# Kernel tuning notes

Hardware: AMD Instinct MI355X
Metric: run time of the kernel (lower is better)

Reference implementation:

```python
import jax, jax.numpy as jnp
import numpy as np

# Marching-tetrahedra lookup tables (identical to the torch module).
_TRI_TABLE = np.array([
    [-1,-1,-1,-1,-1,-1],[1,0,2,-1,-1,-1],[4,0,3,-1,-1,-1],[1,4,2,1,3,4],
    [3,1,5,-1,-1,-1],[2,3,0,2,5,3],[1,4,0,1,5,4],[4,2,5,-1,-1,-1],
    [4,5,2,-1,-1,-1],[4,1,0,4,5,1],[3,2,0,3,5,2],[1,3,5,-1,-1,-1],
    [4,1,2,4,3,1],[3,0,4,-1,-1,-1],[2,0,1,-1,-1,-1],[-1,-1,-1,-1,-1,-1]], dtype=np.int64)
_NUM_TRI = np.array([0,1,1,2,1,2,2,1,1,2,2,1,2,1,1,0], dtype=np.int64)
_BASE_EDGES = np.array([0,1,0,2,0,3,1,2,1,3,2,3], dtype=np.int64)
_NUM_TETS = np.array([0,1,1,3,1,3,3,3,1,3,3,3,3,3,3,1], dtype=np.int64)
_TET_TABLE = np.array([
    [-1,-1,-1,-1,-1,-1,-1,-1,-1,-1,-1,-1],[0,4,5,6,-1,-1,-1,-1,-1,-1,-1,-1],
    [1,4,8,7,-1,-1,-1,-1,-1,-1,-1,-1],[7,1,8,6,5,1,7,6,5,0,1,6],
    [2,5,7,9,-1,-1,-1,-1,-1,-1,-1,-1],[4,0,6,7,9,0,7,6,7,0,9,2],
    [4,1,9,8,5,1,9,4,5,1,2,9],[6,0,1,2,8,6,1,2,9,6,8,2],
    [3,6,9,8,-1,-1,-1,-1,-1,-1,-1,-1],[5,0,4,8,5,0,8,3,5,8,9,3],
    [1,4,7,3,4,7,6,3,9,6,7,3],[0,1,5,3,5,1,9,3,5,1,7,9],
    [5,2,3,7,3,6,5,8,3,5,7,8],[0,4,7,8,0,3,8,7,0,3,7,2],
    [4,1,2,3,4,3,2,5,4,3,5,6],[0,1,2,3,-1,-1,-1,-1,-1,-1,-1,-1]], dtype=np.int64)


def _precompute(n_verts, sdf, tet, thickness):
    """Integer / no_grad half of DMTet.__call__ (dynamic shapes -> host numpy)."""
    sdf = np.asarray(sdf)
    tet = np.asarray(tet).astype(np.int64)
    th = float(np.asarray(thickness).reshape(-1)[0])
    occ = (sdf > 0) & (sdf <= th)                      # [N]
    occ_f = occ[tet]                                   # [F,4]
    occ_sum = occ_f.sum(-1)
    valid = (occ_sum > 0) & (occ_sum < 4)
    vt = tet[valid]                                    # [V,4] surface tets
    edges = vt[:, _BASE_EDGES].reshape(-1, 2)          # [V*6,2]
    edges = np.sort(edges, axis=1)                     # == sort_edges
    uniq, inv = np.unique(edges, axis=0, return_inverse=True)
    inv = inv.reshape(-1)
    mask_e = occ[uniq].sum(-1) == 1                    # crossing edges
    mapping = np.full(uniq.shape[0], -1, dtype=np.int64)
    mapping[mask_e] = np.arange(int(mask_e.sum()), dtype=np.int64)
    idx_map = mapping[inv].reshape(-1, 6)              # [V,6]
    interp_v = uniq[mask_e]                            # [E,2]
    ti = (occ_f[valid].astype(np.int64) * np.array([1, 2, 4, 8])).sum(-1)  # tetindex
    nt = _NUM_TRI[ti]
    f1 = np.take_along_axis(idx_map[nt == 1], _TRI_TABLE[ti[nt == 1]][:, :3], axis=1).reshape(-1, 3)
    f2 = np.take_along_axis(idx_map[nt == 2], _TRI_TABLE[ti[nt == 2]][:, :6], axis=1).reshape(-1, 3)
    faces = np.concatenate([f1, f2], axis=0)
    ntt = _NUM_TETS[ti]
    tve = np.concatenate([vt, idx_map + n_verts], axis=1)  # [V,10]: 4 verts + 6 edge-verts
    t1 = np.take_along_axis(tve[ntt == 1], _TET_TABLE[ti[ntt == 1]][:, :4], axis=1).reshape(-1, 4)
    t3 = np.take_along_axis(tve[ntt == 3], _TET_TABLE[ti[ntt == 3]][:, :12], axis=1).reshape(-1, 4)
    inner = tet[occ_sum == 4]
    all_tets = np.concatenate([t1, t3, inner], axis=0)
    all_unique, inv2 = np.unique(all_tets.reshape(-1), return_inverse=True)
    tets_tetmesh = inv2.reshape(-1, 4)
    return interp_v, faces, all_unique, tets_tetmesh


def _interp(pos, sdf, th, interp_v, all_unique_tets):
    """Differentiable half: edge interpolation + gather of tetmesh verts."""
    e = pos[interp_v.reshape(-1)].reshape(-1, 2, 3)    # [E,2,3]
    s = sdf[interp_v.reshape(-1)].reshape(-1, 2, 1)    # [E,2,1]
    both_pos = (s[:, 0, 0] > 0) & (s[:, 1, 0] > 0)
    s = jnp.where(both_pos[:, None, None], s - th, s)  # shift band edges
    s = s * jnp.array([1.0, -1.0], dtype=s.dtype)[None, :, None]  # negate 2nd
    denom = s.sum(axis=1, keepdims=True)
    w = jnp.flip(s, axis=1) / denom                    # linear interp weights
    verts = (e * w).sum(axis=1)                        # [E,3]
    all_verts = jnp.concatenate([pos, verts], axis=0)
    verts_tetmesh = all_verts[all_unique_tets]
    return verts, verts_tetmesh


def setup_inputs() -> dict:
    key = jax.random.key(0)
    k1, k2, k3, k4 = jax.random.split(key, 4)
    N, F = 400000, 2000000
    pos_nx3 = jax.random.normal(k1, (N, 3), dtype=jnp.float32)
    sdf_n = jax.random.normal(k2, (N,), dtype=jnp.float32)
    tet_fx4 = jax.random.randint(k3, (F, 4), 0, N, dtype=jnp.int32)
    thickness = jax.random.uniform(k4, (1,), dtype=jnp.float32, minval=0.3, maxval=0.8)
    return {"pos_nx3": pos_nx3, "sdf_n": sdf_n, "tet_fx4": tet_fx4, "thickness": thickness}


def reference(pos_nx3, sdf_n, tet_fx4, thickness):
    interp_v, faces, all_unique, tets_tm = _precompute(pos_nx3.shape[0], sdf_n, tet_fx4, thickness)
    verts, verts_tetmesh = _interp(pos_nx3, sdf_n, thickness[0], jnp.asarray(interp_v), jnp.asarray(all_unique))
    return verts, jnp.asarray(faces), verts_tetmesh, jnp.asarray(tets_tm)
```

## Files before the change

kernel.cpp:

```cpp
#include <hip/hip_runtime.h>
#include <stdint.h>

typedef unsigned int u32;
typedef unsigned long long u64;

__device__ __constant__ int c_TRI[16][6] = {
 {-1,-1,-1,-1,-1,-1},{1,0,2,-1,-1,-1},{4,0,3,-1,-1,-1},{1,4,2,1,3,4},
 {3,1,5,-1,-1,-1},{2,3,0,2,5,3},{1,4,0,1,5,4},{4,2,5,-1,-1,-1},
 {4,5,2,-1,-1,-1},{4,1,0,4,5,1},{3,2,0,3,5,2},{1,3,5,-1,-1,-1},
 {4,1,2,4,3,1},{3,0,4,-1,-1,-1},{2,0,1,-1,-1,-1},{-1,-1,-1,-1,-1,-1}};
__device__ __constant__ int c_NTRI[16] = {0,1,1,2,1,2,2,1,1,2,2,1,2,1,1,0};
__device__ __constant__ int c_NTET[16] = {0,1,1,3,1,3,3,3,1,3,3,3,3,3,3,1};
__device__ __constant__ int c_TET[16][12] = {
 {-1,-1,-1,-1,-1,-1,-1,-1,-1,-1,-1,-1},{0,4,5,6,-1,-1,-1,-1,-1,-1,-1,-1},
 {1,4,8,7,-1,-1,-1,-1,-1,-1,-1,-1},{7,1,8,6,5,1,7,6,5,0,1,6},
 {2,5,7,9,-1,-1,-1,-1,-1,-1,-1,-1},{4,0,6,7,9,0,7,6,7,0,9,2},
 {4,1,9,8,5,1,9,4,5,1,2,9},{6,0,1,2,8,6,1,2,9,6,8,2},
 {3,6,9,8,-1,-1,-1,-1,-1,-1,-1,-1},{5,0,4,8,5,0,8,3,5,8,9,3},
 {1,4,7,3,4,7,6,3,9,6,7,3},{0,1,5,3,5,1,9,3,5,1,7,9},
 {5,2,3,7,3,6,5,8,3,5,7,8},{0,4,7,8,0,3,8,7,0,3,7,2},
 {4,1,2,3,4,3,2,5,4,3,5,6},{0,1,2,3,-1,-1,-1,-1,-1,-1,-1,-1}};
__device__ __constant__ int c_EV[12] = {0,1,0,2,0,3,1,2,1,3,2,3};

#define GSLOOP(i,n) for (long long i = (long long)blockIdx.x*blockDim.x + threadIdx.x; \
                         i < (long long)(n); i += (long long)gridDim.x*blockDim.x)

__global__ __launch_bounds__(256) void k_scan1(u32* data, u32* partials,
                                               const u32* hdr, int nslot, u32 nmax) {
  __shared__ u32 lds[2048];
  __shared__ u32 tsum[256];
  u32 n = (nslot >= 0) ? hdr[nslot] : nmax;
  u32 base = blockIdx.x * 2048u;
  for (int k = threadIdx.x; k < 2048; k += 256) {
    u32 i = base + (u32)k;
    lds[k] = (i < n) ? data[i] : 0u;
  }
  __syncthreads();
  u32 o = threadIdx.x * 8u;
  u32 run = 0; u32 loc[8];
  #pragma unroll
  for (int j = 0; j < 8; j++) { loc[j] = run; run += lds[o + j]; }
  tsum[threadIdx.x] = run;
  __syncthreads();
  for (int off = 1; off < 256; off <<= 1) {
    u32 v = tsum[threadIdx.x];
    u32 add = (threadIdx.x >= (u32)off) ? tsum[threadIdx.x - off] : 0u;
    __syncthreads();
    tsum[threadIdx.x] = v + add;
    __syncthreads();
  }
  u32 texc = (threadIdx.x == 0) ? 0u : tsum[threadIdx.x - 1];
  #pragma unroll
  for (int j = 0; j < 8; j++) {
    u32 i = base + o + (u32)j;
    if (i < n) data[i] = texc + loc[j];
  }
  if (threadIdx.x == 0) partials[blockIdx.x] = tsum[255];
}

__global__ __launch_bounds__(1024) void k_scan2(u32* partials, const u32* hdr, int nslot,
                                                u32 nmax, u32* hdrw, int tslot) {
  __shared__ u32 lds[8192];
  __shared__ u32 tsum[1024];
  u32 n = (nslot >= 0) ? hdr[nslot] : nmax;
  u32 nb = (n + 2047u) / 2048u;
  for (int k = threadIdx.x; k < 8192; k += 1024) lds[k] = ((u32)k < nb) ? partials[k] : 0u;
  __syncthreads();
  u32 o = threadIdx.x * 8u;
  u32 run = 0; u32 loc[8];
  #pragma unroll
  for (int j = 0; j < 8; j++) { loc[j] = run; run += lds[o + j]; }
  tsum[threadIdx.x] = run;
  __syncthreads();
  for (int off = 1; off < 1024; off <<= 1) {
    u32 v = tsum[threadIdx.x];
    u32 add = (threadIdx.x >= (u32)off) ? tsum[threadIdx.x - off] : 0u;
    __syncthreads();
    tsum[threadIdx.x] = v + add;
    __syncthreads();
  }
  u32 texc = (threadIdx.x == 0) ? 0u : tsum[threadIdx.x - 1];
  #pragma unroll
  for (int j = 0; j < 8; j++) { u32 k = o + (u32)j; if (k < nb) partials[k] = texc + loc[j]; }
  if (threadIdx.x == 0 && tslot >= 0) hdrw[tslot] = tsum[1023];
}

__global__ __launch_bounds__(256) void k_scan3(u32* data, const u32* partials,
                                               const u32* hdr, int nslot, u32 nmax) {
  u32 n = (nslot >= 0) ? hdr[nslot] : nmax;
  u32 base = blockIdx.x * 2048u;
  if (base >= n || blockIdx.x == 0) return;
  u32 add = partials[blockIdx.x];
  if (add == 0) return;
  for (int k = threadIdx.x; k < 2048; k += 256) {
    u32 i = base + (u32)k;
    if (i < n) data[i] += add;
  }
}

__global__ void k_zero32(u32* p, long long n) { GSLOOP(i, n) p[i] = 0u; }
__global__ void k_zero_hdr(u32* p, const u32* hdr, int slot, u32 extra) {
  long long n = (long long)hdr[slot] + extra;
  GSLOOP(i, n) p[i] = 0u;
}
__global__ void k_copy32(const u32* s, u32* d, long long n) { GSLOOP(i, n) d[i] = s[i]; }
__global__ void k_setr(u32* hdr, int N) { hdr[10] = (u32)N + hdr[3]; }

__global__ void k_occ(const float* sdf, const float* th, unsigned char* occ, int N) {
  float t = th[0];
  GSLOOP(i, N) { float s = sdf[i]; occ[i] = (s > 0.f && s <= t) ? 1 : 0; }
}

__global__ void k_ti(const int* tet, const unsigned char* occ, unsigned char* ti,
                     u32* S1, long long F) {
  GSLOOP(f, F) {
    int v0 = tet[4*f], v1 = tet[4*f+1], v2 = tet[4*f+2], v3 = tet[4*f+3];
    int b = (int)occ[v0] | ((int)occ[v1] << 1) | ((int)occ[v2] << 2) | ((int)occ[v3] << 3);
    ti[f] = (unsigned char)b;
    S1[f] = (b != 0 && b != 15) ? 1u : 0u;
  }
}

__global__ void k_compact_valid(const u32* S1, const unsigned char* ti, u32* vidx, long long F) {
  GSLOOP(f, F) { int b = ti[f]; if (b != 0 && b != 15) vidx[S1[f]] = (u32)f; }
}

__global__ void k_hist(const int* tet, const u32* vidx, const u32* hdr, u32* hist) {
  u32 V = hdr[0];
  GSLOOP(t, V) {
    long long f = vidx[t];
    int v[4] = { tet[4*f], tet[4*f+1], tet[4*f+2], tet[4*f+3] };
    #pragma unroll
    for (int e = 0; e < 6; e++) {
      int a = v[c_EV[2*e]], b = v[c_EV[2*e+1]];
      int mn = a < b ? a : b;
      atomicAdd(&hist[mn], 1u);
    }
  }
}

__global__ void k_bnd(const u32* off, u32* hdr, int N) {
  int g = threadIdx.x;
  if (g > 8) return;
  if (g == 8) { hdr[16 + 8] = (u32)N; return; }
  u64 target = ((u64)hdr[1] * (u64)g) / 8ull;
  u32 lo = 0, hi = (u32)N;
  while (lo < hi) { u32 m = (lo + hi) >> 1; if ((u64)off[m] < target) lo = m + 1; else hi = m; }
  hdr[16 + g] = lo;
}

__global__ void k_scatter8(const int* tet, const u32* vidx, const u32* hdr,
                           u32* cursor, u64* keys, int SB, int OB) {
  int g = blockIdx.x & 7;
  u32 lo = hdr[16 + g], hi = hdr[16 + g + 1];
  u32 V = hdr[0];
  for (long long t = (long long)(blockIdx.x >> 3) * blockDim.x + threadIdx.x; t < (long long)V;
       t += (long long)(gridDim.x >> 3) * blockDim.x) {
    long long f = vidx[t];
    int v[4] = { tet[4*f], tet[4*f+1], tet[4*f+2], tet[4*f+3] };
    #pragma unroll
    for (int e = 0; e < 6; e++) {
      int a = v[c_EV[2*e]], b = v[c_EV[2*e+1]];
      int mn = a < b ? a : b, mx = a < b ? b : a;
      if ((u32)mn >= lo && (u32)mn < hi) {
        u32 p = atomicAdd(&cursor[mn], 1u);
        keys[p] = (((u64)(u32)mn << (SB + OB)) | ((u64)(u32)mx << OB)) | (u64)(6ull * t + e);
      }
    }
  }
}

template<int KMAX>
__device__ __forceinline__ void bitonic_lane(u64& val, int lane) {
  #pragma unroll
  for (int k = 2; k <= KMAX; k <<= 1) {
    #pragma unroll
    for (int j = k >> 1; j > 0; j >>= 1) {
      u64 other = __shfl_xor(val, j, 64);
      bool keepmin = ((lane & k) == 0) == ((lane & j) == 0);
      bool smaller = val < other;
      val = (keepmin == smaller) ? val : other;
    }
  }
}

__global__ __launch_bounds__(256) void k_bsort(const u32* off, u64* keys, u32* cfe,
                                               const unsigned char* occm, int N,
                                               int SB, int OB) {
  int lane = threadIdx.x & 63;
  u64 smask = ((u64)1 << SB) - 1;
  long long wid = ((long long)blockIdx.x * blockDim.x + threadIdx.x) >> 6;
  long long nw  = ((long long)gridDim.x * blockDim.x) >> 6;
  for (long long v = wid; v < N; v += nw) {
    u32 s = off[v], e = off[v + 1];
    u32 cnt = e - s;
    if (cnt == 0) continue;
    int ov = (int)occm[v];
    if (cnt == 1) {
      if (lane == 0) {
        u32 mx = (u32)((keys[s] >> OB) & smask);
        cfe[s] = ((ov + (int)occm[mx]) == 1) ? 1u : 0u;
      }
      continue;
    }
    if (cnt <= 64) {
      u64 val = (lane < (int)cnt) ? keys[s + lane] : ~0ull;
      if      (cnt <= 2)  bitonic_lane<2>(val, lane);
      else if (cnt <= 4)  bitonic_lane<4>(val, lane);
      else if (cnt <= 8)  bitonic_lane<8>(val, lane);
      else if (cnt <= 16) bitonic_lane<16>(val, lane);
      else if (cnt <= 32) bitonic_lane<32>(val, lane);
      else                bitonic_lane<64>(val, lane);
      u64 prev = __shfl_up(val, 1, 64);
      if (lane < (int)cnt) {
        keys[s + lane] = val;
        bool flag = (lane == 0) || ((val >> OB) != (prev >> OB));
        u32 mx = (u32)((val >> OB) & smask);
        cfe[s + lane] = (flag && ((ov + (int)occm[mx]) == 1)) ? 1u : 0u;
      }
    } else if (cnt <= 256) {
      u64 vals[4];
      #pragma unroll
      for (int r = 0; r < 4; r++) {
        int idx = r * 64 + lane;
        vals[r] = (idx < (int)cnt) ? keys[s + idx] : ~0ull;
      }
      #pragma unroll
      for (int k = 2; k <= 256; k <<= 1) {
        #pragma unroll
        for (int j = 128; j > 0; j >>= 1) {
          if (j >= k) continue;
          if (j >= 64) {
            int rj = j >> 6;
            #pragma unroll
            for (int r = 0; r < 4; r++) {
              int pr = r ^ rj;
              if (pr > r) {
                int i0 = r * 64 + lane;
                bool keepmin = ((i0 & k) == 0);
                u64 a = vals[r], b = vals[pr];
                u64 mn = a < b ? a : b, mx = a < b ? b : a;
                vals[r]  = keepmin ? mn : mx;
                vals[pr] = keepmin ? mx : mn;
              }
            }
          } else {
            #pragma unroll
            for (int r = 0; r < 4; r++) {
              int i0 = r * 64 + lane;
              u64 other = __shfl_xor(vals[r], j, 64);
              bool keepmin = ((i0 & k) == 0) == ((i0 & j) == 0);
              bool smaller = vals[r] < other;
              vals[r] = (keepmin == smaller) ? vals[r] : other;
            }
          }
        }
      }
      #pragma unroll
      for (int r = 0; r < 4; r++) {
        u64 pv = __shfl_up(vals[r], 1, 64);
        u64 lastprev = (r > 0) ? __shfl(vals[r - 1], 63, 64) : 0ull;
        int idx = r * 64 + lane;
        u64 prev = (lane == 0) ? lastprev : pv;
        if (idx < (int)cnt) {
          keys[s + idx] = vals[r];
          bool flag = (idx == 0) || ((vals[r] >> OB) != (prev >> OB));
          u32 mx = (u32)((vals[r] >> OB) & smask);
          cfe[s + idx] = (flag && ((ov + (int)occm[mx]) == 1)) ? 1u : 0u;
        }
      }
    } else if (lane == 0) {
      for (u32 i = s + 1; i < e; i++) {
        u64 kk = keys[i]; u32 j = i;
        while (j > s && keys[j - 1] > kk) { keys[j] = keys[j - 1]; j--; }
        keys[j] = kk;
      }
      for (u32 j = s; j < e; j++) {
        bool flag = (j == s) || ((keys[j] >> OB) != (keys[j - 1] >> OB));
        u32 mx = (u32)((keys[j] >> OB) & smask);
        cfe[j] = (flag && ((ov + (int)occm[mx]) == 1)) ? 1u : 0u;
      }
    }
  }
}

__global__ void k_idxscatter8(const u64* keys, const u32* S, const unsigned char* occm,
                              int* idx_map, u64* ie, const u32* hdr, int SB, int OB) {
  u32 E = hdr[1];
  int g = blockIdx.x & 7;
  u64 omask = ((u64)1 << OB) - 1;
  u64 smask = ((u64)1 << SB) - 1;
  for (long long i = (long long)(blockIdx.x >> 3) * blockDim.x + threadIdx.x; i < (long long)E;
       i += (long long)(gridDim.x >> 3) * blockDim.x) {
    u64 k = keys[i];
    u32 oidx = (u32)(k & omask);
    u32 mx = (u32)((k >> OB) & smask);
    u32 mn = (u32)(k >> (SB + OB));
    bool flag = (i == 0) || ((k >> OB) != (keys[i - 1] >> OB));
    bool cf = ((int)occm[mn] + (int)occm[mx]) == 1;
    u32 sv = S[i];
    int mapval = cf ? (int)(flag ? sv : sv - 1u) : -1;
    u32 slice = (u32)(((u64)oidx * 8ull) / (u64)E);
    if (slice == (u32)g) idx_map[oidx] = mapval;
    if (g == 0 && flag && cf) ie[sv] = ((u64)mn << 32) | (u64)mx;
  }
}

__global__ void k_interp(const u64* ie, const float* pos, const float* sdf,
                         const float* th, float* out, const u32* hdr) {
  u32 EC = hdr[3];
  float t = th[0];
  GSLOOP(m, EC) {
    u64 k = ie[m]; int a = (int)(k >> 32), b = (int)(k & 0xffffffffu);
    float s0 = sdf[a], s1 = sdf[b];
    if (s0 > 0.f && s1 > 0.f) { s0 = __fsub_rn(s0, t); s1 = __fsub_rn(s1, t); }
    float denom = __fadd_rn(s0, -s1);
    float w0 = __fdiv_rn(-s1, denom);
    float w1 = __fdiv_rn(s0, denom);
    long long base = 3ll * m;
    #pragma unroll
    for (int kk = 0; kk < 3; kk++)
      out[base + kk] = __fadd_rn(__fmul_rn(pos[3ll*a + kk], w0), __fmul_rn(pos[3ll*b + kk], w1));
  }
}

__global__ void k_pred_faces(const unsigned char* ti, u32* S1, u32* S2, long long F) {
  GSLOOP(f, F) {
    int b = ti[f]; bool valid = (b != 0 && b != 15); int nt = c_NTRI[b];
    S1[f] = (valid && nt == 1) ? 1u : 0u;
    S2[f] = (valid && nt == 2) ? 1u : 0u;
  }
}

__global__ void k_faces(const u32* vidx, const unsigned char* ti, const int* idx_map,
                        const u32* S1, const u32* S2, float* out, const u32* hdr) {
  u32 V = hdr[0];
  unsigned long long fo = 3ull * hdr[3];
  u32 Nf1 = hdr[4];
  GSLOOP(t, V) {
    u32 f = vidx[t]; int b = ti[f]; int nt = c_NTRI[b];
    if (nt == 1) {
      unsigned long long base = fo + 3ull * S1[f];
      for (int k = 0; k < 3; k++) out[base + k] = (float)idx_map[6*t + c_TRI[b][k]];
    } else {
      unsigned long long base = fo + 3ull * Nf1 + 6ull * S2[f];
      for (int k = 0; k < 6; k++) out[base + k] = (float)idx_map[6*t + c_TRI[b][k]];
    }
  }
}

__global__ void k_pred_tets(const unsigned char* ti, u32* S1, u32* S2, u32* S3, long long F) {
  GSLOOP(f, F) {
    int b = ti[f]; bool valid = (b != 0 && b != 15); int ntt = c_NTET[b];
    S1[f] = (valid && ntt == 1) ? 1u : 0u;
    S2[f] = (valid && ntt == 3) ? 1u : 0u;
    S3[f] = (b == 15) ? 1u : 0u;
  }
}

__global__ void k_tets_valid(const int* tet, const u32* vidx, const unsigned char* ti,
                             const int* idx_map, const u32* S1, const u32* S2,
                             int* at, const u32* hdr, int N) {
  u32 V = hdr[0]; u32 Nt1 = hdr[6];
  GSLOOP(t, V) {
    u32 f = vidx[t]; int b = ti[f];
    int tv[10];
    for (int k = 0; k < 4; k++) tv[k] = tet[4ll*f + k];
    for (int j = 0; j < 6; j++) tv[4 + j] = idx_map[6*t + j] + N;
    int ntt = c_NTET[b];
    if (ntt == 1) {
      long long base = 4ll * S1[f];
      for (int k = 0; k < 4; k++) at[base + k] = tv[c_TET[b][k]];
    } else {
      long long base = 4ll * Nt1 + 12ll * S2[f];
      for (int k = 0; k < 12; k++) at[base + k] = tv[c_TET[b][k]];
    }
  }
}

__global__ void k_tets_inner(const int* tet, const unsigned char* ti, const u32* S3,
                             int* at, const u32* hdr, long long F) {
  long long base0 = 4ll * hdr[6] + 12ll * hdr[7];
  GSLOOP(f, F) {
    if (ti[f] == 15) {
      long long base = base0 + 4ll * S3[f];
      for (int k = 0; k < 4; k++) at[base + k] = tet[4*f + k];
    }
  }
}

__global__ void k_mark(const int* at, u32* Big, const u32* hdr) {
  long long NA = 4ll * hdr[6] + 12ll * hdr[7] + 4ll * hdr[8];
  GSLOOP(i, NA) Big[at[i]] = 1u;
}

__global__ void k_vtm(const u32* Big, const float* pos, float* out, const u32* hdr, int N) {
  u32 R = hdr[10], NU = hdr[9];
  unsigned long long vtm = 3ull * hdr[3] + 3ull * (hdr[4] + 2u * hdr[5]);
  GSLOOP(v, R) {
    u32 r = Big[v];
    u32 nx = (v + 1 < (long long)R) ? Big[v + 1] : NU;
    if (nx > r) {
      unsigned long long base = vtm + 3ull * r;
      if (v < N) { for (int k = 0; k < 3; k++) out[base + k] = pos[3*v + k]; }
      else { long long src = 3ll * (v - N); for (int k = 0; k < 3; k++) out[base + k] = out[src + k]; }
    }
  }
}

__global__ void k_tets_out(const int* at, const u32* Big, float* out, const u32* hdr) {
  long long NA = 4ll * hdr[6] + 12ll * hdr[7] + 4ll * hdr[8];
  unsigned long long toff = 3ull * hdr[3] + 3ull * (hdr[4] + 2u * hdr[5]) + 3ull * hdr[9];
  GSLOOP(i, NA) out[toff + i] = (float)Big[at[i]];
}

extern "C" void kernel_launch(void* const* d_in, const int* in_sizes, int n_in,
                              void* d_out, int out_size, void* d_ws, size_t ws_size,
                              hipStream_t stream) {
  const float* pos = (const float*)d_in[0];
  const float* sdf = (const float*)d_in[1];
  const int*   tet = (const int*)d_in[2];
  const float* th  = (const float*)d_in[3];
  float* out = (float*)d_out;

  const int N = in_sizes[1];
  const long long F = (long long)in_sizes[2] / 4;
  const long long MAXE = 6 * F;
  const long long RMAX = (long long)N + MAXE;
  (void)n_in; (void)out_size; (void)ws_size;

  int SB = 1; while ((1ll << SB) < (long long)N) SB++;
  int OB = 1; while ((1ll << OB) < MAXE) OB++;

  char* w = (char*)d_ws;
  size_t off = 0;
  auto alloc = [&](size_t b) -> char* {
    char* p = w + off; off = (off + b + 255) & ~(size_t)255; return p;
  };
  u32* hdr            = (u32*)alloc(64 * 4);
  unsigned char* occ  = (unsigned char*)alloc((size_t)N);
  unsigned char* tiA  = (unsigned char*)alloc((size_t)F);
  u32* S1             = (u32*)alloc(4 * (size_t)F);
  u32* S2             = (u32*)alloc(4 * (size_t)F);
  u32* S3             = (u32*)alloc(4 * (size_t)F);
  u32* vidx           = (u32*)alloc(4 * (size_t)F);
  u32* hist           = (u32*)alloc(4 * ((size_t)N + 2));
  u32* cursor         = (u32*)alloc(4 * ((size_t)N + 2));
  char* big_mem       = alloc(8 * (size_t)MAXE);
  u64* keys = (u64*)big_mem; int* at = (int*)big_mem;
  u64* ie             = (u64*)alloc(8 * (size_t)MAXE);
  u32* Big            = (u32*)alloc(4 * ((size_t)RMAX + 2));
  u32* cfe            = (u32*)alloc(4 * (size_t)MAXE);
  int* idx_map        = (int*)alloc(4 * (size_t)MAXE);
  u32* partials       = (u32*)alloc(4 * 8192);

  const int GRID = 4096, BLK = 256;
  auto scan = [&](u32* data, int nslot, u32 nmax, int tslot) {
    int nb = (int)((nmax + 2047u) / 2048u);
    k_scan1<<<nb, 256, 0, stream>>>(data, partials, hdr, nslot, nmax);
    k_scan2<<<1, 1024, 0, stream>>>(partials, hdr, nslot, nmax, hdr, tslot);
    k_scan3<<<nb, 256, 0, stream>>>(data, partials, hdr, nslot, nmax);
  };

  k_zero32<<<1, 64, 0, stream>>>(hdr, 64);
  k_zero32<<<2048, BLK, 0, stream>>>(hist, (long long)N + 2);

  k_occ<<<GRID, BLK, 0, stream>>>(sdf, th, occ, N);
  k_ti<<<GRID, BLK, 0, stream>>>(tet, occ, tiA, S1, F);
  scan(S1, -1, (u32)F, 0);
  k_compact_valid<<<GRID, BLK, 0, stream>>>(S1, tiA, vidx, F);

  k_hist<<<GRID, BLK, 0, stream>>>(tet, vidx, hdr, hist);
  scan(hist, -1, (u32)(N + 1), 1);
  k_bnd<<<1, 64, 0, stream>>>(hist, hdr, N);
  k_copy32<<<GRID, BLK, 0, stream>>>(hist, cursor, (long long)N + 2);
  k_scatter8<<<GRID, BLK, 0, stream>>>(tet, vidx, hdr, cursor, keys, SB, OB);
  k_bsort<<<GRID, BLK, 0, stream>>>(hist, keys, cfe, occ, N, SB, OB);

  scan(cfe, 1, (u32)MAXE, 3);
  k_setr<<<1, 1, 0, stream>>>(hdr, N);
  k_idxscatter8<<<GRID, BLK, 0, stream>>>(keys, cfe, occ, idx_map, ie, hdr, SB, OB);

  k_interp<<<GRID, BLK, 0, stream>>>(ie, pos, sdf, th, out, hdr);

  k_pred_faces<<<GRID, BLK, 0, stream>>>(tiA, S1, S2, F);
  scan(S1, -1, (u32)F, 4);
  scan(S2, -1, (u32)F, 5);
  k_faces<<<GRID, BLK, 0, stream>>>(vidx, tiA, idx_map, S1, S2, out, hdr);

  k_pred_tets<<<GRID, BLK, 0, stream>>>(tiA, S1, S2, S3, F);
  scan(S1, -1, (u32)F, 6);
  scan(S2, -1, (u32)F, 7);
  scan(S3, -1, (u32)F, 8);
  k_tets_valid<<<GRID, BLK, 0, stream>>>(tet, vidx, tiA, idx_map, S1, S2, at, hdr, N);
  k_tets_inner<<<GRID, BLK, 0, stream>>>(tet, tiA, S3, at, hdr, F);

  k_zero_hdr<<<GRID, BLK, 0, stream>>>(Big, hdr, 10, 2u);
  k_mark<<<GRID, BLK, 0, stream>>>(at, Big, hdr);
  scan(Big, 10, (u32)RMAX, 9);
  k_vtm<<<GRID, BLK, 0, stream>>>(Big, pos, out, hdr, N);
  k_tets_out<<<GRID, BLK, 0, stream>>>(at, Big, out, hdr);
}
```

Baseline: 1.622 ms.

## Materialize edge keys once, scatter in 32 slices, fuse rank/interp and face/tet emission

Edge keys are now built and stored once in the histogram pass. The scatter reads them linearly in four rounds of eight bucket slices, instead of re-gathering tets for every slice. The sort kernel computes per-vertex crossing-edge counts and local ranks with ballot/popcount, so the large MAXE-length scan over cfe becomes an N-length scan. Interpolation is fused into the rank pass, and the face and tet predicate and emit kernels are merged. This adds extra erec/lrv/oix/mv buffers and more scatter launches, and Big now aliases the erec buffer.

```diff
diff --git a/kernel.cpp b/kernel.cpp
--- a/kernel.cpp
+++ b/kernel.cpp
@@ -125,7 +125,8 @@
   GSLOOP(f, F) { int b = ti[f]; if (b != 0 && b != 15) vidx[S1[f]] = (u32)f; }
 }
 
-__global__ void k_hist(const int* tet, const u32* vidx, const u32* hdr, u32* hist) {
+__global__ void k_edges(const int* tet, const u32* vidx, const u32* hdr,
+                        u32* hist, u64* erec, int SB, int OB) {
   u32 V = hdr[0];
   GSLOOP(t, V) {
     long long f = vidx[t];
@@ -133,39 +134,37 @@
     #pragma unroll
     for (int e = 0; e < 6; e++) {
       int a = v[c_EV[2*e]], b = v[c_EV[2*e+1]];
-      int mn = a < b ? a : b;
+      int mn = a < b ? a : b, mx = a < b ? b : a;
       atomicAdd(&hist[mn], 1u);
-    }
-  }
-}
-
-__global__ void k_bnd(const u32* off, u32* hdr, int N) {
+      u64 key = (((u64)(u32)mn << (SB + OB)) | ((u64)(u32)mx << OB)) | (u64)(6ull * t + e);
+      __builtin_nontemporal_store(key, &erec[6ll * t + e]);
+    }
+  }
+}
+
+__global__ void k_bnd32(const u32* off, const u32* hdr, u32* bnd, int N) {
   int g = threadIdx.x;
-  if (g > 8) return;
-  if (g == 8) { hdr[16 + 8] = (u32)N; return; }
-  u64 target = ((u64)hdr[1] * (u64)g) / 8ull;
+  if (g > 32) return;
+  if (g == 32) { bnd[32] = (u32)N; return; }
+  u64 target = ((u64)hdr[1] * (u64)g) / 32ull;
   u32 lo = 0, hi = (u32)N;
   while (lo < hi) { u32 m = (lo + hi) >> 1; if ((u64)off[m] < target) lo = m + 1; else hi = m; }
-  hdr[16 + g] = lo;
-}
-
-__global__ void k_scatter8(const int* tet, const u32* vidx, const u32* hdr,
-                           u32* cursor, u64* keys, int SB, int OB) {
+  bnd[g] = lo;
+}
+
+__global__ void k_scatter32(const u64* erec, const u32* bnd, const u32* hdr,
+                            u32* cursor, u64* keys, int SB, int OB, int round) {
   int g = blockIdx.x & 7;
-  u32 lo = hdr[16 + g], hi = hdr[16 + g + 1];
-  u32 V = hdr[0];
-  for (long long t = (long long)(blockIdx.x >> 3) * blockDim.x + threadIdx.x; t < (long long)V;
-       t += (long long)(gridDim.x >> 3) * blockDim.x) {
-    long long f = vidx[t];
-    int v[4] = { tet[4*f], tet[4*f+1], tet[4*f+2], tet[4*f+3] };
-    #pragma unroll
-    for (int e = 0; e < 6; e++) {
-      int a = v[c_EV[2*e]], b = v[c_EV[2*e+1]];
-      int mn = a < b ? a : b, mx = a < b ? b : a;
-      if ((u32)mn >= lo && (u32)mn < hi) {
-        u32 p = atomicAdd(&cursor[mn], 1u);
-        keys[p] = (((u64)(u32)mn << (SB + OB)) | ((u64)(u32)mx << OB)) | (u64)(6ull * t + e);
-      }
+  int sidx = round * 8 + g;
+  u32 lo = bnd[sidx], hi = bnd[sidx + 1];
+  u32 E = hdr[1];
+  for (long long i = (long long)(blockIdx.x >> 3) * blockDim.x + threadIdx.x; i < (long long)E;
+       i += (long long)(gridDim.x >> 3) * blockDim.x) {
+    u64 k = __builtin_nontemporal_load(&erec[i]);
+    u32 mn = (u32)(k >> (SB + OB));
+    if (mn >= lo && mn < hi) {
+      u32 p = atomicAdd(&cursor[mn], 1u);
+      keys[p] = k;
     }
   }
 }
@@ -184,22 +183,25 @@
   }
 }
 
-__global__ __launch_bounds__(256) void k_bsort(const u32* off, u64* keys, u32* cfe,
-                                               const unsigned char* occm, int N,
+__global__ __launch_bounds__(256) void k_bsort(const u32* off, u64* keys, u32* lrv,
+                                               u32* bc, const unsigned char* occm, int N,
                                                int SB, int OB) {
   int lane = threadIdx.x & 63;
   u64 smask = ((u64)1 << SB) - 1;
+  u64 ltm = (lane == 0) ? 0ull : (~0ull >> (64 - lane));
   long long wid = ((long long)blockIdx.x * blockDim.x + threadIdx.x) >> 6;
   long long nw  = ((long long)gridDim.x * blockDim.x) >> 6;
   for (long long v = wid; v < N; v += nw) {
     u32 s = off[v], e = off[v + 1];
     u32 cnt = e - s;
-    if (cnt == 0) continue;
+    if (cnt == 0) { if (lane == 0) bc[v] = 0u; continue; }
     int ov = (int)occm[v];
     if (cnt == 1) {
       if (lane == 0) {
         u32 mx = (u32)((keys[s] >> OB) & smask);
-        cfe[s] = ((ov + (int)occm[mx]) == 1) ? 1u : 0u;
+        u32 cf = ((ov + (int)occm[mx]) == 1) ? 1u : 0u;
+        lrv[s] = (cf << 31) | (1u << 30);
+        bc[v] = cf;
       }
       continue;
     }
@@ -212,12 +214,17 @@
       else if (cnt <= 32) bitonic_lane<32>(val, lane);
       else                bitonic_lane<64>(val, lane);
       u64 prev = __shfl_up(val, 1, 64);
-      if (lane < (int)cnt) {
+      bool inb = lane < (int)cnt;
+      bool flag = inb && (lane == 0 || (val >> OB) != (prev >> OB));
+      u32 mx = (u32)((val >> OB) & smask);
+      bool cf = inb && ((ov + (int)occm[mx]) == 1);
+      u64 m = __ballot(flag && cf);
+      u32 lr = (u32)__popcll(m & ltm);
+      if (inb) {
         keys[s + lane] = val;
-        bool flag = (lane == 0) || ((val >> OB) != (prev >> OB));
-        u32 mx = (u32)((val >> OB) & smask);
-        cfe[s + lane] = (flag && ((ov + (int)occm[mx]) == 1)) ? 1u : 0u;
-      }
+        lrv[s + lane] = (cf ? 0x80000000u : 0u) | (flag ? 0x40000000u : 0u) | lr;
+      }
+      if (lane == 0) bc[v] = (u32)__popcll(m);
     } else if (cnt <= 256) {
       u64 vals[4];
       #pragma unroll
@@ -256,134 +263,151 @@
           }
         }
       }
+      bool flags[4], cfs[4]; u64 masks[4];
       #pragma unroll
       for (int r = 0; r < 4; r++) {
         u64 pv = __shfl_up(vals[r], 1, 64);
         u64 lastprev = (r > 0) ? __shfl(vals[r - 1], 63, 64) : 0ull;
         int idx = r * 64 + lane;
         u64 prev = (lane == 0) ? lastprev : pv;
+        bool inb = idx < (int)cnt;
+        flags[r] = inb && (idx == 0 || (vals[r] >> OB) != (prev >> OB));
+        u32 mx = (u32)((vals[r] >> OB) & smask);
+        cfs[r] = inb && ((ov + (int)occm[mx]) == 1);
+        masks[r] = __ballot(flags[r] && cfs[r]);
+      }
+      u32 base = 0;
+      #pragma unroll
+      for (int r = 0; r < 4; r++) {
+        u32 lr = base + (u32)__popcll(masks[r] & ltm);
+        int idx = r * 64 + lane;
         if (idx < (int)cnt) {
           keys[s + idx] = vals[r];
-          bool flag = (idx == 0) || ((vals[r] >> OB) != (prev >> OB));
-          u32 mx = (u32)((vals[r] >> OB) & smask);
-          cfe[s + idx] = (flag && ((ov + (int)occm[mx]) == 1)) ? 1u : 0u;
+          lrv[s + idx] = (cfs[r] ? 0x80000000u : 0u) | (flags[r] ? 0x40000000u : 0u) | lr;
         }
-      }
+        base += (u32)__popcll(masks[r]);
+      }
+      if (lane == 0) bc[v] = base;
     } else if (lane == 0) {
       for (u32 i = s + 1; i < e; i++) {
         u64 kk = keys[i]; u32 j = i;
         while (j > s && keys[j - 1] > kk) { keys[j] = keys[j - 1]; j--; }
         keys[j] = kk;
       }
+      u32 lr = 0;
       for (u32 j = s; j < e; j++) {
         bool flag = (j == s) || ((keys[j] >> OB) != (keys[j - 1] >> OB));
         u32 mx = (u32)((keys[j] >> OB) & smask);
-        cfe[j] = (flag && ((ov + (int)occm[mx]) == 1)) ? 1u : 0u;
-      }
-    }
-  }
-}
-
-__global__ void k_idxscatter8(const u64* keys, const u32* S, const unsigned char* occm,
-                              int* idx_map, u64* ie, const u32* hdr, int SB, int OB) {
+        bool cf = ((ov + (int)occm[mx]) == 1);
+        lrv[j] = (cf ? 0x80000000u : 0u) | (flag ? 0x40000000u : 0u) | lr;
+        if (flag && cf) lr++;
+      }
+      bc[v] = lr;
+    }
+  }
+}
+
+__global__ void k_ie_interp(const u64* keys, const u32* lrv, const u32* bc0,
+                            const float* pos, const float* sdf, const float* th,
+                            u32* oix, int* mv, float* out, const u32* hdr, int SB, int OB) {
+  u32 E = hdr[1];
+  float t = th[0];
+  u64 omask = ((u64)1 << OB) - 1;
+  u64 smask = ((u64)1 << SB) - 1;
+  GSLOOP(i, E) {
+    u64 k = __builtin_nontemporal_load(&keys[i]);
+    u32 l = __builtin_nontemporal_load(&lrv[i]);
+    u32 oidx = (u32)(k & omask);
+    bool cf = (l >> 31) & 1, flag = (l >> 30) & 1;
+    u32 lr = l & 0x3fffffffu;
+    int mapv = -1;
+    if (cf) {
+      u32 mn = (u32)(k >> (SB + OB));
+      u32 rank = bc0[mn] + lr - (flag ? 0u : 1u);
+      mapv = (int)rank;
+      if (flag) {
+        int a = (int)mn, b = (int)(u32)((k >> OB) & smask);
+        float s0 = sdf[a], s1 = sdf[b];
+        if (s0 > 0.f && s1 > 0.f) { s0 = __fsub_rn(s0, t); s1 = __fsub_rn(s1, t); }
+        float denom = __fadd_rn(s0, -s1);
+        float w0 = __fdiv_rn(-s1, denom);
+        float w1 = __fdiv_rn(s0, denom);
+        long long base = 3ll * rank;
+        #pragma unroll
+        for (int kk = 0; kk < 3; kk++)
+          out[base + kk] = __fadd_rn(__fmul_rn(pos[3ll*a + kk], w0), __fmul_rn(pos[3ll*b + kk], w1));
+      }
+    }
+    __builtin_nontemporal_store(oidx, &oix[i]);
+    __builtin_nontemporal_store(mapv, &mv[i]);
+  }
+}
+
+__global__ void k_fin(const u32* oix, const int* mv, int* idx_map, const u32* hdr) {
   u32 E = hdr[1];
   int g = blockIdx.x & 7;
-  u64 omask = ((u64)1 << OB) - 1;
-  u64 smask = ((u64)1 << SB) - 1;
   for (long long i = (long long)(blockIdx.x >> 3) * blockDim.x + threadIdx.x; i < (long long)E;
        i += (long long)(gridDim.x >> 3) * blockDim.x) {
-    u64 k = keys[i];
-    u32 oidx = (u32)(k & omask);
-    u32 mx = (u32)((k >> OB) & smask);
-    u32 mn = (u32)(k >> (SB + OB));
-    bool flag = (i == 0) || ((k >> OB) != (keys[i - 1] >> OB));
-    bool cf = ((int)occm[mn] + (int)occm[mx]) == 1;
-    u32 sv = S[i];
-    int mapval = cf ? (int)(flag ? sv : sv - 1u) : -1;
-    u32 slice = (u32)(((u64)oidx * 8ull) / (u64)E);
-    if (slice == (u32)g) idx_map[oidx] = mapval;
-    if (g == 0 && flag && cf) ie[sv] = ((u64)mn << 32) | (u64)mx;
-  }
-}
-
-__global__ void k_interp(const u64* ie, const float* pos, const float* sdf,
-                         const float* th, float* out, const u32* hdr) {
-  u32 EC = hdr[3];
-  float t = th[0];
-  GSLOOP(m, EC) {
-    u64 k = ie[m]; int a = (int)(k >> 32), b = (int)(k & 0xffffffffu);
-    float s0 = sdf[a], s1 = sdf[b];
-    if (s0 > 0.f && s1 > 0.f) { s0 = __fsub_rn(s0, t); s1 = __fsub_rn(s1, t); }
-    float denom = __fadd_rn(s0, -s1);
-    float w0 = __fdiv_rn(-s1, denom);
-    float w1 = __fdiv_rn(s0, denom);
-    long long base = 3ll * m;
-    #pragma unroll
-    for (int kk = 0; kk < 3; kk++)
-      out[base + kk] = __fadd_rn(__fmul_rn(pos[3ll*a + kk], w0), __fmul_rn(pos[3ll*b + kk], w1));
-  }
-}
-
-__global__ void k_pred_faces(const unsigned char* ti, u32* S1, u32* S2, long long F) {
+    u32 o = __builtin_nontemporal_load(&oix[i]);
+    int m = __builtin_nontemporal_load(&mv[i]);
+    u32 slice = (u32)(((u64)o * 8ull) / (u64)E);
+    if (slice == (u32)g) idx_map[o] = m;
+  }
+}
+
+__global__ void k_predall(const unsigned char* ti, u32* Sf1, u32* Sf2,
+                          u32* St1, u32* St3, u32* Si, long long F) {
   GSLOOP(f, F) {
-    int b = ti[f]; bool valid = (b != 0 && b != 15); int nt = c_NTRI[b];
-    S1[f] = (valid && nt == 1) ? 1u : 0u;
-    S2[f] = (valid && nt == 2) ? 1u : 0u;
-  }
-}
-
-__global__ void k_faces(const u32* vidx, const unsigned char* ti, const int* idx_map,
-                        const u32* S1, const u32* S2, float* out, const u32* hdr) {
+    int b = ti[f]; bool valid = (b != 0 && b != 15);
+    int nt = c_NTRI[b]; int ntt = c_NTET[b];
+    Sf1[f] = (valid && nt == 1) ? 1u : 0u;
+    Sf2[f] = (valid && nt == 2) ? 1u : 0u;
+    St1[f] = (valid && ntt == 1) ? 1u : 0u;
+    St3[f] = (valid && ntt == 3) ? 1u : 0u;
+    Si[f]  = (b == 15) ? 1u : 0u;
+  }
+}
+
+__global__ void k_emit_ft(const int* tet, const u32* vidx, const unsigned char* ti,
+                          const int* idx_map, const u32* Sf1, const u32* Sf2,
+                          const u32* St1, const u32* St3, float* out, int* at,
+                          const u32* hdr, int N) {
   u32 V = hdr[0];
   unsigned long long fo = 3ull * hdr[3];
-  u32 Nf1 = hdr[4];
-  GSLOOP(t, V) {
-    u32 f = vidx[t]; int b = ti[f]; int nt = c_NTRI[b];
-    if (nt == 1) {
-      unsigned long long base = fo + 3ull * S1[f];
-      for (int k = 0; k < 3; k++) out[base + k] = (float)idx_map[6*t + c_TRI[b][k]];
-    } else {
-      unsigned long long base = fo + 3ull * Nf1 + 6ull * S2[f];
-      for (int k = 0; k < 6; k++) out[base + k] = (float)idx_map[6*t + c_TRI[b][k]];
-    }
-  }
-}
-
-__global__ void k_pred_tets(const unsigned char* ti, u32* S1, u32* S2, u32* S3, long long F) {
-  GSLOOP(f, F) {
-    int b = ti[f]; bool valid = (b != 0 && b != 15); int ntt = c_NTET[b];
-    S1[f] = (valid && ntt == 1) ? 1u : 0u;
-    S2[f] = (valid && ntt == 3) ? 1u : 0u;
-    S3[f] = (b == 15) ? 1u : 0u;
-  }
-}
-
-__global__ void k_tets_valid(const int* tet, const u32* vidx, const unsigned char* ti,
-                             const int* idx_map, const u32* S1, const u32* S2,
-                             int* at, const u32* hdr, int N) {
-  u32 V = hdr[0]; u32 Nt1 = hdr[6];
+  u32 Nf1 = hdr[4], Nt1 = hdr[6];
   GSLOOP(t, V) {
     u32 f = vidx[t]; int b = ti[f];
+    int im[6];
+    #pragma unroll
+    for (int j = 0; j < 6; j++) im[j] = idx_map[6*t + j];
+    int nt = c_NTRI[b];
+    if (nt == 1) {
+      unsigned long long base = fo + 3ull * Sf1[f];
+      for (int k = 0; k < 3; k++) out[base + k] = (float)im[c_TRI[b][k]];
+    } else {
+      unsigned long long base = fo + 3ull * Nf1 + 6ull * Sf2[f];
+      for (int k = 0; k < 6; k++) out[base + k] = (float)im[c_TRI[b][k]];
+    }
     int tv[10];
     for (int k = 0; k < 4; k++) tv[k] = tet[4ll*f + k];
-    for (int j = 0; j < 6; j++) tv[4 + j] = idx_map[6*t + j] + N;
+    for (int j = 0; j < 6; j++) tv[4 + j] = im[j] + N;
     int ntt = c_NTET[b];
     if (ntt == 1) {
-      long long base = 4ll * S1[f];
+      long long base = 4ll * St1[f];
       for (int k = 0; k < 4; k++) at[base + k] = tv[c_TET[b][k]];
     } else {
-      long long base = 4ll * Nt1 + 12ll * S2[f];
+      long long base = 4ll * Nt1 + 12ll * St3[f];
       for (int k = 0; k < 12; k++) at[base + k] = tv[c_TET[b][k]];
     }
   }
 }
 
-__global__ void k_tets_inner(const int* tet, const unsigned char* ti, const u32* S3,
+__global__ void k_tets_inner(const int* tet, const unsigned char* ti, const u32* Si,
                              int* at, const u32* hdr, long long F) {
   long long base0 = 4ll * hdr[6] + 12ll * hdr[7];
   GSLOOP(f, F) {
     if (ti[f] == 15) {
-      long long base = base0 + 4ll * S3[f];
+      long long base = base0 + 4ll * Si[f];
       for (int k = 0; k < 4; k++) at[base + k] = tet[4*f + k];
     }
   }
@@ -438,19 +462,25 @@
     char* p = w + off; off = (off + b + 255) & ~(size_t)255; return p;
   };
   u32* hdr            = (u32*)alloc(64 * 4);
+  u32* bnd            = (u32*)alloc(64 * 4);
   unsigned char* occ  = (unsigned char*)alloc((size_t)N);
   unsigned char* tiA  = (unsigned char*)alloc((size_t)F);
   u32* S1             = (u32*)alloc(4 * (size_t)F);
   u32* S2             = (u32*)alloc(4 * (size_t)F);
   u32* S3             = (u32*)alloc(4 * (size_t)F);
+  u32* S4             = (u32*)alloc(4 * (size_t)F);
+  u32* S5             = (u32*)alloc(4 * (size_t)F);
   u32* vidx           = (u32*)alloc(4 * (size_t)F);
   u32* hist           = (u32*)alloc(4 * ((size_t)N + 2));
   u32* cursor         = (u32*)alloc(4 * ((size_t)N + 2));
-  char* big_mem       = alloc(8 * (size_t)MAXE);
-  u64* keys = (u64*)big_mem; int* at = (int*)big_mem;
-  u64* ie             = (u64*)alloc(8 * (size_t)MAXE);
-  u32* Big            = (u32*)alloc(4 * ((size_t)RMAX + 2));
-  u32* cfe            = (u32*)alloc(4 * (size_t)MAXE);
+  u32* bc             = (u32*)alloc(4 * ((size_t)N + 2));
+  char* erec_mem      = alloc(8 * (size_t)MAXE);
+  u64* erec = (u64*)erec_mem; u32* Big = (u32*)erec_mem;
+  char* keys_mem      = alloc(8 * (size_t)MAXE);
+  u64* keys = (u64*)keys_mem; int* at = (int*)keys_mem;
+  u32* lrv            = (u32*)alloc(4 * (size_t)MAXE);
+  u32* oix            = (u32*)alloc(4 * (size_t)MAXE);
+  int* mv             = (int*)alloc(4 * (size_t)MAXE);
   int* idx_map        = (int*)alloc(4 * (size_t)MAXE);
   u32* partials       = (u32*)alloc(4 * 8192);
 
@@ -470,30 +500,27 @@
   scan(S1, -1, (u32)F, 0);
   k_compact_valid<<<GRID, BLK, 0, stream>>>(S1, tiA, vidx, F);
 
-  k_hist<<<GRID, BLK, 0, stream>>>(tet, vidx, hdr, hist);
+  k_edges<<<GRID, BLK, 0, stream>>>(tet, vidx, hdr, hist, erec, SB, OB);
   scan(hist, -1, (u32)(N + 1), 1);
-  k_bnd<<<1, 64, 0, stream>>>(hist, hdr, N);
+  k_bnd32<<<1, 64, 0, stream>>>(hist, hdr, bnd, N);
   k_copy32<<<GRID, BLK, 0, stream>>>(hist, cursor, (long long)N + 2);
-  k_scatter8<<<GRID, BLK, 0, stream>>>(tet, vidx, hdr, cursor, keys, SB, OB);
-  k_bsort<<<GRID, BLK, 0, stream>>>(hist, keys, cfe, occ, N, SB, OB);
-
-  scan(cfe, 1, (u32)MAXE, 3);
+  for (int r = 0; r < 4; r++)
+    k_scatter32<<<GRID, BLK, 0, stream>>>(erec, bnd, hdr, cursor, keys, SB, OB, r);
+  k_bsort<<<GRID, BLK, 0, stream>>>(hist, keys, lrv, bc, occ, N, SB, OB);
+
+  scan(bc, -1, (u32)N, 3);
   k_setr<<<1, 1, 0, stream>>>(hdr, N);
-  k_idxscatter8<<<GRID, BLK, 0, stream>>>(keys, cfe, occ, idx_map, ie, hdr, SB, OB);
-
-  k_interp<<<GRID, BLK, 0, stream>>>(ie, pos, sdf, th, out, hdr);
-
-  k_pred_faces<<<GRID, BLK, 0, stream>>>(tiA, S1, S2, F);
+  k_ie_interp<<<GRID, BLK, 0, stream>>>(keys, lrv, bc, pos, sdf, th, oix, mv, out, hdr, SB, OB);
+  k_fin<<<GRID, BLK, 0, stream>>>(oix, mv, idx_map, hdr);
+
+  k_predall<<<GRID, BLK, 0, stream>>>(tiA, S1, S2, S3, S4, S5, F);
   scan(S1, -1, (u32)F, 4);
   scan(S2, -1, (u32)F, 5);
-  k_faces<<<GRID, BLK, 0, stream>>>(vidx, tiA, idx_map, S1, S2, out, hdr);
-
-  k_pred_tets<<<GRID, BLK, 0, stream>>>(tiA, S1, S2, S3, F);
-  scan(S1, -1, (u32)F, 6);
-  scan(S2, -1, (u32)F, 7);
-  scan(S3, -1, (u32)F, 8);
-  k_tets_valid<<<GRID, BLK, 0, stream>>>(tet, vidx, tiA, idx_map, S1, S2, at, hdr, N);
-  k_tets_inner<<<GRID, BLK, 0, stream>>>(tet, tiA, S3, at, hdr, F);
+  scan(S3, -1, (u32)F, 6);
+  scan(S4, -1, (u32)F, 7);
+  scan(S5, -1, (u32)F, 8);
+  k_emit_ft<<<GRID, BLK, 0, stream>>>(tet, vidx, tiA, idx_map, S1, S2, S3, S4, out, at, hdr, N);
+  k_tets_inner<<<GRID, BLK, 0, stream>>>(tet, tiA, S5, at, hdr, F);
 
   k_zero_hdr<<<GRID, BLK, 0, stream>>>(Big, hdr, 10, 2u);
   k_mark<<<GRID, BLK, 0, stream>>>(at, Big, hdr);
```

New measurement: 1.630 ms. No clear change (+0.5%).
